# Kernel optimization log

Measured on AMD Instinct MI355X. Metric: run time of the kernel, lower is better.

Reference implementation:

```python
import jax, jax.numpy as jnp
import numpy as np
import math

B, N, DEG, C, F0, NCLS = 128, 512, 8, 128, 128, 10
E = B * N * DEG
RATIO = 0.8
K1 = math.ceil(RATIO * N)    # 410
K2 = math.ceil(RATIO * K1)   # 328
K3 = math.ceil(RATIO * K2)   # 263


def setup_inputs() -> dict:
    key = jax.random.key(0)
    ks = jax.random.split(key, 32)
    x = jax.random.normal(ks[0], (B * N, F0), jnp.float32)
    epg = N * DEG
    src_l = jax.random.randint(ks[1], (B, epg), 0, N)
    dst_l = jax.random.randint(ks[2], (B, epg), 0, N)
    off = (jnp.arange(B, dtype=jnp.int32) * N)[:, None]
    edge_src = (src_l + off).reshape(-1).astype(jnp.int32)
    edge_dst = (dst_l + off).reshape(-1).astype(jnp.int32)

    def lin(k, fi, fo):
        return jax.random.normal(k, (fi, fo), jnp.float32) / np.float32(np.sqrt(fi))

    inp = {"x": x, "edge_src": edge_src, "edge_dst": edge_dst}
    i = 3
    for s, fi in (("1", F0), ("2", C), ("3", C)):
        inp["Wroot" + s] = lin(ks[i], fi, C); i += 1
        inp["Wrel" + s] = lin(ks[i], fi, C); i += 1
        inp["brel" + s] = jnp.zeros((C,), jnp.float32)
        inp["p" + s] = jax.random.normal(ks[i], (C,), jnp.float32); i += 1
    inp["W1"] = lin(ks[i], 2 * C, 128); i += 1
    inp["b1"] = jnp.zeros((128,), jnp.float32)
    inp["W2"] = lin(ks[i], 128, 64); i += 1
    inp["b2"] = jnp.zeros((64,), jnp.float32)
    inp["W3"] = lin(ks[i], 64, NCLS); i += 1
    inp["b3"] = jnp.zeros((NCLS,), jnp.float32)
    return inp


def graph_conv(x, src, dst, emask, Wroot, Wrel, brel, num_nodes):
    # PyG GraphConv (aggr='add'): lin_rel(sum_j x_j) + lin_root(x_i)
    msg = x[src] * emask[:, None]                      # masked gather  [E, C]
    agg = jax.ops.segment_sum(msg, dst, num_segments=num_nodes)
    return agg @ Wrel + brel + x @ Wroot


def topk_pool(x, p, src, dst, emask, b, n, k):
    # score = tanh(x . p / ||p||), keep top-k nodes per graph, scale kept x by score
    score = jnp.tanh((x @ p) / jnp.linalg.norm(p))     # [b*n]
    vals, idx = jax.lax.top_k(score.reshape(b, n), k)  # [b, k]
    perm = (idx + (jnp.arange(b, dtype=idx.dtype) * n)[:, None]).reshape(-1)
    x_new = x[perm] * vals.reshape(-1, 1)
    inv = jnp.full((b * n,), -1, jnp.int32).at[perm].set(
        jnp.arange(b * k, dtype=jnp.int32))
    ns, nd = inv[src], inv[dst]
    nmask = emask * (ns >= 0) * (nd >= 0)
    return x_new, jnp.maximum(ns, 0), jnp.maximum(nd, 0), nmask


def readout(h, b, k):
    hb = h.reshape(b, k, -1)
    return jnp.concatenate([hb.max(axis=1), hb.mean(axis=1)], axis=-1)  # gmp||gap


def reference(x, edge_src, edge_dst,
              Wroot1, Wrel1, brel1, p1,
              Wroot2, Wrel2, brel2, p2,
              Wroot3, Wrel3, brel3, p3,
              W1, b1, W2, b2, W3, b3):
    emask = jnp.ones((E,), x.dtype)
    s, d = edge_src, edge_dst

    h = jax.nn.relu(graph_conv(x, s, d, emask, Wroot1, Wrel1, brel1, B * N))
    h, s, d, emask = topk_pool(h, p1, s, d, emask, B, N, K1)
    x1 = readout(h, B, K1)

    h = jax.nn.relu(graph_conv(h, s, d, emask, Wroot2, Wrel2, brel2, B * K1))
    h, s, d, emask = topk_pool(h, p2, s, d, emask, B, K1, K2)
    x2 = readout(h, B, K2)

    h = jax.nn.relu(graph_conv(h, s, d, emask, Wroot3, Wrel3, brel3, B * K2))
    h, s, d, emask = topk_pool(h, p3, s, d, emask, B, K2, K3)
    x3 = readout(h, B, K3)

    g = x1 + x2 + x3                                   # [B, 256]
    g = jax.nn.relu(g @ W1 + b1)                       # dropout is identity in eval
    g = jax.nn.relu(g @ W2 + b2)
    return jax.nn.log_softmax(g @ W3 + b3, axis=-1)    # [B, NCLS]
```

## Files before the change

kernel.cpp:

```cpp
#include <hip/hip_runtime.h>
#include <hip/hip_bf16.h>
#include <math.h>

#define B_G   128
#define N0    512
#define DEG   8
#define CCH   128
#define EPG   (N0*DEG)
#define E_TOTAL (B_G*EPG)
#define K1    410
#define K2    328
#define K3    263
#define NCLS  10

#define SWZ(row, cb) ((((cb) ^ ((row) & 7)) << 2))

using bf16x8 = __attribute__((ext_vector_type(8))) __bf16;
using f32x4  = __attribute__((ext_vector_type(4))) float;
typedef unsigned short ushort;
typedef unsigned int uint;
typedef unsigned long long u64;

__device__ __forceinline__ ushort f2b(float f) {
    uint u = __float_as_uint(f);
    u += 0x7fffu + ((u >> 16) & 1u);
    return (ushort)(u >> 16);
}
__device__ __forceinline__ float b2f(ushort h) {
    return __uint_as_float(((uint)h) << 16);
}
__device__ __forceinline__ void split2(float v, ushort& hi, ushort& lo) {
    hi = f2b(v);
    lo = f2b(v - b2f(hi));
}
__device__ __forceinline__ uint pksplit(float v) {
    ushort h, l; split2(v, h, l);
    return (uint)h | ((uint)l << 16);
}
__device__ __forceinline__ float unpk(uint u) {
    return __uint_as_float(u << 16) + __uint_as_float(u & 0xffff0000u);
}
__device__ __forceinline__ float keyval(u64 key) {
    uint tu = (uint)(key >> 32);
    uint su = (tu & 0x80000000u) ? (tu & 0x7fffffffu) : ~tu;
    return __uint_as_float(su);
}

__global__ __launch_bounds__(512) void setup_kernel(
        const float* __restrict__ Wrel0, const float* __restrict__ Wroot0,
        const float* __restrict__ Wrel1, const float* __restrict__ Wroot1,
        const float* __restrict__ Wrel2, const float* __restrict__ Wroot2,
        ushort* __restrict__ Bph, ushort* __restrict__ Bpl,
        const int* __restrict__ es, const int* __restrict__ ed,
        int* __restrict__ indptr0, int* __restrict__ counts0, ushort* __restrict__ srclist0) {
    __shared__ uint epk[EPG];
    __shared__ int cnt[512], pref[512], curs[512];
    if (blockIdx.x < B_G) {
        int b = blockIdx.x, tid = threadIdx.x;
        cnt[tid] = 0;
        __syncthreads();
        int base = b * EPG;
        for (int i = tid; i < EPG; i += 512) {
            int s = es[base + i] & (N0 - 1);
            int d = ed[base + i] & (N0 - 1);
            epk[i] = (uint)s | ((uint)d << 16);
            atomicAdd(&cnt[d], 1);
        }
        __syncthreads();
        pref[tid] = cnt[tid];
        __syncthreads();
        for (int off = 1; off < 512; off <<= 1) {
            int v = (tid >= off) ? pref[tid - off] : 0;
            __syncthreads();
            pref[tid] += v;
            __syncthreads();
        }
        int excl = tid ? pref[tid - 1] : 0;
        indptr0[b * N0 + tid] = base + excl;
        counts0[b * N0 + tid] = cnt[tid];
        curs[tid] = excl;
        __syncthreads();
        for (int i = tid; i < EPG; i += 512) {
            uint wv = epk[i];
            int dl = wv >> 16;
            int pos = atomicAdd(&curs[dl], 1);
            srclist0[base + pos] = (ushort)(wv & 0xFFFFu);
        }
    } else {
        int i = (blockIdx.x - B_G) * 512 + threadIdx.x;
        if (i < 3 * 32768) {
            int layer = i >> 15, rem = i & 32767;
            int j = rem & 7, lane = (rem >> 3) & 63, cf = (rem >> 9) & 7, ks = rem >> 12;
            int k = ks * 32 + (lane >> 4) * 8 + j;
            int c = cf * 16 + (lane & 15);
            const float* Wrel  = layer == 0 ? Wrel0  : layer == 1 ? Wrel1  : Wrel2;
            const float* Wroot = layer == 0 ? Wroot0 : layer == 1 ? Wroot1 : Wroot2;
            float v = (k < 128) ? Wrel[k * 128 + c] : Wroot[(k - 128) * 128 + c];
            ushort hi, lo; split2(v, hi, lo);
            Bph[i] = hi; Bpl[i] = lo;
        }
    }
}

__global__ __launch_bounds__(1024) void aggregate0(
        const float* __restrict__ xf,
        const int* __restrict__ indptr, const int* __restrict__ counts,
        const ushort* __restrict__ srclist,
        uint* __restrict__ aggp) {
    extern __shared__ float slab[];
    int b = blockIdx.x >> 2, q = blockIdx.x & 3;
    int tid = threadIdx.x;
    const float4* xf4 = (const float4*)xf;
    for (int t = tid; t < N0 * 8; t += 1024) {
        int nd = t >> 3, c4 = t & 7;
        float4 u = xf4[(size_t)(b * N0 + nd) * 32 + q * 8 + c4];
        *(float4*)&slab[nd * 32 + SWZ(nd, c4)] = u;
    }
    __syncthreads();
    int wave = tid >> 6, lane = tid & 63;
    int gl = lane >> 3, sub = lane & 7;
    for (int g = wave; g < N0 / 8; g += 16) {
        int d = g * 8 + gl;
        int beg = indptr[b * N0 + d];
        int cnt = counts[b * N0 + d];
        float4 acc = make_float4(0.f, 0.f, 0.f, 0.f);
        int id_next = (cnt > 0) ? (int)srclist[beg] : 0;
        for (int j = 0; j < cnt; j++) {
            int id = id_next;
            if (j + 1 < cnt) id_next = (int)srclist[beg + j + 1];
            const float4 v = *(const float4*)&slab[id * 32 + SWZ(id, sub)];
            acc.x += v.x; acc.y += v.y; acc.z += v.z; acc.w += v.w;
        }
        uint4 o;
        o.x = pksplit(acc.x); o.y = pksplit(acc.y);
        o.z = pksplit(acc.z); o.w = pksplit(acc.w);
        *(uint4*)&aggp[(size_t)(b * N0 + d) * CCH + q * 32 + sub * 4] = o;
    }
}

__global__ __launch_bounds__(512, 4) void transform_mfma(
        const uint* __restrict__ aggp, const uint* __restrict__ rootp,
        const float* __restrict__ rootf, const float* __restrict__ sval,
        const ushort* __restrict__ Bph, const ushort* __restrict__ Bpl,
        const float* __restrict__ brel, const float* __restrict__ pvec,
        uint* __restrict__ hout, float* __restrict__ score) {
    __shared__ ushort ldsBh[16384];
    __shared__ ushort ldsBl[16384];
    int tid = threadIdx.x;
    int wave = tid >> 6, lane = tid & 63;
    int r = lane & 15, kb = lane >> 4;
    int rows0 = blockIdx.x * 128 + wave * 16;
    int gid = rows0 + r;
    float rv = sval ? sval[gid] : 1.f;

    f32x4 acc[8];
#pragma unroll
    for (int cf = 0; cf < 8; cf++) acc[cf] = (f32x4)(0.f);

    union U16 { uint u[4]; bf16x8 v; };

#pragma unroll
    for (int half = 0; half < 2; half++) {
        if (half) __syncthreads();
#pragma unroll
        for (int i = 0; i < 4; i++) {
            int idx = tid + i * 512;
            ((uint4*)ldsBh)[idx] = ((const uint4*)(Bph + half * 16384))[idx];
            ((uint4*)ldsBl)[idx] = ((const uint4*)(Bpl + half * 16384))[idx];
        }
        __syncthreads();
#pragma unroll
        for (int ks4 = 0; ks4 < 4; ks4++) {
            U16 ah, al;
            if (half && rootf) {
                const float* R = rootf + (size_t)gid * CCH + ks4 * 32 + kb * 8;
                float4 f0 = *(const float4*)R;
                float4 f1 = *(const float4*)(R + 4);
                float c[8] = {f0.x, f0.y, f0.z, f0.w, f1.x, f1.y, f1.z, f1.w};
#pragma unroll
                for (int p2 = 0; p2 < 4; p2++) {
                    ushort h0, l0, h1, l1;
                    split2(c[2 * p2], h0, l0);
                    split2(c[2 * p2 + 1], h1, l1);
                    ah.u[p2] = (uint)h0 | ((uint)h1 << 16);
                    al.u[p2] = (uint)l0 | ((uint)l1 << 16);
                }
            } else {
                const uint* A = half ? rootp : aggp;
                size_t rowbase = (size_t)gid * CCH + ks4 * 32 + kb * 8;
                uint4 ua = *(const uint4*)&A[rowbase];
                uint4 ub = *(const uint4*)&A[rowbase + 4];
                if (half && sval) {
                    float c[8] = {unpk(ua.x) * rv, unpk(ua.y) * rv, unpk(ua.z) * rv,
                                  unpk(ua.w) * rv, unpk(ub.x) * rv, unpk(ub.y) * rv,
                                  unpk(ub.z) * rv, unpk(ub.w) * rv};
#pragma unroll
                    for (int p2 = 0; p2 < 4; p2++) {
                        ushort h0, l0, h1, l1;
                        split2(c[2 * p2], h0, l0);
                        split2(c[2 * p2 + 1], h1, l1);
                        ah.u[p2] = (uint)h0 | ((uint)h1 << 16);
                        al.u[p2] = (uint)l0 | ((uint)l1 << 16);
                    }
                } else {
                    ah.u[0] = (ua.x & 0xffffu) | (ua.y << 16);
                    ah.u[1] = (ua.z & 0xffffu) | (ua.w << 16);
                    ah.u[2] = (ub.x & 0xffffu) | (ub.y << 16);
                    ah.u[3] = (ub.z & 0xffffu) | (ub.w << 16);
                    al.u[0] = (ua.x >> 16) | (ua.y & 0xffff0000u);
                    al.u[1] = (ua.z >> 16) | (ua.w & 0xffff0000u);
                    al.u[2] = (ub.x >> 16) | (ub.y & 0xffff0000u);
                    al.u[3] = (ub.z >> 16) | (ub.w & 0xffff0000u);
                }
            }
#pragma unroll
            for (int cf = 0; cf < 8; cf++) {
                bf16x8 bh = *(const bf16x8*)&ldsBh[((ks4 * 8 + cf) * 64 + lane) * 8];
                bf16x8 bl = *(const bf16x8*)&ldsBl[((ks4 * 8 + cf) * 64 + lane) * 8];
                acc[cf] = __builtin_amdgcn_mfma_f32_16x16x32_bf16(ah.v, bl, acc[cf], 0, 0, 0);
                acc[cf] = __builtin_amdgcn_mfma_f32_16x16x32_bf16(al.v, bh, acc[cf], 0, 0, 0);
                acc[cf] = __builtin_amdgcn_mfma_f32_16x16x32_bf16(ah.v, bh, acc[cf], 0, 0, 0);
            }
        }
    }

    float pv[8], bb[8], q = 0.f;
#pragma unroll
    for (int cf = 0; cf < 8; cf++) {
        pv[cf] = pvec[cf * 16 + r];
        bb[cf] = brel[cf * 16 + r];
        q += pv[cf] * pv[cf];
    }
    float dots[4] = {0.f, 0.f, 0.f, 0.f};
#pragma unroll
    for (int cf = 0; cf < 8; cf++) {
#pragma unroll
        for (int reg = 0; reg < 4; reg++) {
            float v = acc[cf][reg] + bb[cf];
            v = v > 0.f ? v : 0.f;
            hout[(size_t)(rows0 + kb * 4 + reg) * CCH + cf * 16 + r] = pksplit(v);
            dots[reg] += v * pv[cf];
        }
    }
#pragma unroll
    for (int off = 1; off < 16; off <<= 1) {
        q += __shfl_xor(q, off);
#pragma unroll
        for (int reg = 0; reg < 4; reg++) dots[reg] += __shfl_xor(dots[reg], off);
    }
    if (r == 0) {
        float inv_norm = rsqrtf(q);
#pragma unroll
        for (int reg = 0; reg < 4; reg++)
            score[rows0 + kb * 4 + reg] = tanhf(dots[reg] * inv_norm);
    }
}

__global__ __launch_bounds__(1024) void pool_kernel(
        const float* __restrict__ score, const uint* __restrict__ hp,
        float* __restrict__ gpart,
        const int* __restrict__ ipt, const int* __restrict__ cnt,
        const ushort* __restrict__ srcl,
        const int* __restrict__ valid_in,
        int* __restrict__ valid_out,
        float* __restrict__ sval_out,
        uint* __restrict__ aggout,
        int k) {
    int b = blockIdx.x >> 2, q = blockIdx.x & 3;
    int tid = threadIdx.x;
    __shared__ char selm[512];
    __shared__ float sval[512];
    __shared__ int hist[256];
    __shared__ int cum[257];
    __shared__ int bc[1];
    __shared__ float redbuf[2048];
    extern __shared__ float slab[];

    u64 key = 0ull;
    if (tid < 512) {
        bool v = (!valid_in) || (valid_in[b * N0 + tid] != 0);
        if (v) {
            uint u = __float_as_uint(score[b * N0 + tid]);
            u = (u & 0x80000000u) ? ~u : (u | 0x80000000u);
            key = ((u64)u << 32) | (uint)(~tid);
            sval[tid] = keyval(key);
        }
    }
    for (int t = tid; t < N0 * 8; t += 1024) {
        int nd = t >> 3, c4 = t & 7;
        bool v = (!valid_in) || (valid_in[b * N0 + nd] != 0);
        if (v) {
            uint4 u = *(const uint4*)&hp[(size_t)(b * N0 + nd) * CCH + q * 32 + c4 * 4];
            *(float4*)&slab[nd * 32 + SWZ(nd, c4)] =
                make_float4(unpk(u.x), unpk(u.y), unpk(u.z), unpk(u.w));
        }
    }
    bool active = (tid < 512) && (key != 0ull), sure = false;
    int rem = k;
    for (int pass = 0; pass < 8; pass++) {
        int dig = (int)((key >> (56 - 8 * pass)) & 255);
        if (tid < 256) hist[tid] = 0;
        __syncthreads();
        if (active) atomicAdd(&hist[dig], 1);
        __syncthreads();
        if (tid < 64) {
            int b0 = hist[tid * 4], b1 = hist[tid * 4 + 1];
            int b2 = hist[tid * 4 + 2], b3 = hist[tid * 4 + 3];
            int s = b0 + b1 + b2 + b3;
            int suf = s;
#pragma unroll
            for (int o = 1; o < 64; o <<= 1) {
                int t2 = __shfl_down(suf, o);
                if (tid + o < 64) suf += t2;
            }
            int after = suf - s;
            cum[tid * 4 + 3] = after + b3;
            cum[tid * 4 + 2] = after + b3 + b2;
            cum[tid * 4 + 1] = after + b3 + b2 + b1;
            cum[tid * 4 + 0] = after + s;
            if (tid == 0) cum[256] = 0;
        }
        __syncthreads();
        if (tid < 256 && cum[tid] >= rem && cum[tid + 1] < rem) bc[0] = tid;
        __syncthreads();
        int dstar = bc[0];
        int hcnt = hist[dstar];
        rem -= cum[dstar + 1];
        if (active) {
            if (dig > dstar) { sure = true; active = false; }
            else if (dig < dstar) active = false;
        }
        __syncthreads();
        if (hcnt == 1) break;
    }
    bool sel = sure || (active && rem > 0);
    if (tid < 512) selm[tid] = sel ? 1 : 0;
    __syncthreads();
    for (int t = tid; t < N0 * 8; t += 1024) {
        int nd = t >> 3, c4 = t & 7;
        if (selm[nd]) {
            float v = sval[nd];
            float* p = &slab[nd * 32 + SWZ(nd, c4)];
            p[0] *= v; p[1] *= v; p[2] *= v; p[3] *= v;
        }
    }
    __syncthreads();
    {
        int w = tid >> 5, ch = tid & 31;
        int cb = ch >> 2, ce = ch & 3;
        float mx = -1e30f, sm = 0.f;
        for (int nd = w; nd < N0; nd += 32) {
            float v = slab[nd * 32 + SWZ(nd, cb) + ce];
            if (selm[nd]) { mx = fmaxf(mx, v); sm += v; }
        }
        redbuf[w * 32 + ch] = mx;
        redbuf[1024 + w * 32 + ch] = sm;
    }
    __syncthreads();
    if (tid < 32) {
        float m = -1e30f, s = 0.f;
        for (int w = 0; w < 32; w++) {
            m = fmaxf(m, redbuf[w * 32 + tid]);
            s += redbuf[1024 + w * 32 + tid];
        }
        gpart[b * 256 + q * 32 + tid] = m;
        gpart[b * 256 + 128 + q * 32 + tid] = s / (float)k;
    }
    if (!valid_out) return;
    if (q == 0 && tid < 512) {
        valid_out[b * N0 + tid] = selm[tid] ? 1 : 0;
        sval_out[b * N0 + tid] = selm[tid] ? sval[tid] : 0.f;
    }
    {
        int wave = tid >> 6, lane = tid & 63;
        int gl = lane >> 3, sub = lane & 7;
        for (int g = wave; g < N0 / 8; g += 16) {
            int d = g * 8 + gl;
            bool act = selm[d] != 0;
            int beg = 0, cc = 0;
            if (act) { beg = ipt[b * N0 + d]; cc = cnt[b * N0 + d]; }
            float4 acc = make_float4(0.f, 0.f, 0.f, 0.f);
            int s_next = (cc > 0) ? (int)srcl[beg] : 0;
            for (int j = 0; j < cc; j++) {
                int s = s_next;
                if (j + 1 < cc) s_next = (int)srcl[beg + j + 1];
                if (selm[s]) {
                    const float4 v = *(const float4*)&slab[s * 32 + SWZ(s, sub)];
                    acc.x += v.x; acc.y += v.y; acc.z += v.z; acc.w += v.w;
                }
            }
            if (act) {
                uint4 o;
                o.x = pksplit(acc.x); o.y = pksplit(acc.y);
                o.z = pksplit(acc.z); o.w = pksplit(acc.w);
                *(uint4*)&aggout[(size_t)(b * N0 + d) * CCH + q * 32 + sub * 4] = o;
            }
        }
    }
}

__global__ __launch_bounds__(128) void mlp_kernel(const float* __restrict__ gpart,
        const float* __restrict__ W1, const float* __restrict__ b1,
        const float* __restrict__ W2, const float* __restrict__ b2,
        const float* __restrict__ W3, const float* __restrict__ b3,
        float* __restrict__ out) {
    int b = blockIdx.x, t = threadIdx.x;
    __shared__ float gs[256], h1[128], h2[64], lg[10];
    const float* g0 = gpart + ((size_t)0 * B_G + b) * 256;
    const float* g1 = gpart + ((size_t)1 * B_G + b) * 256;
    const float* g2 = gpart + ((size_t)2 * B_G + b) * 256;
    gs[t] = g0[t] + g1[t] + g2[t];
    gs[128 + t] = g0[128 + t] + g1[128 + t] + g2[128 + t];
    __syncthreads();
    {
        float a = b1[t];
        for (int c = 0; c < 256; c++) a += gs[c] * W1[c * 128 + t];
        h1[t] = fmaxf(a, 0.f);
    }
    __syncthreads();
    if (t < 64) {
        float a = b2[t];
        for (int c = 0; c < 128; c++) a += h1[c] * W2[c * 64 + t];
        h2[t] = fmaxf(a, 0.f);
    }
    __syncthreads();
    if (t < 10) {
        float a = b3[t];
        for (int c = 0; c < 64; c++) a += h2[c] * W3[c * 10 + t];
        lg[t] = a;
    }
    __syncthreads();
    if (t < 10) {
        float m = lg[0];
        for (int i = 1; i < 10; i++) m = fmaxf(m, lg[i]);
        float s = 0.f;
        for (int i = 0; i < 10; i++) s += expf(lg[i] - m);
        out[b * 10 + t] = lg[t] - m - logf(s);
    }
}

extern "C" void kernel_launch(void* const* d_in, const int* in_sizes, int n_in,
                              void* d_out, int out_size, void* d_ws, size_t ws_size,
                              hipStream_t stream) {
    (void)in_sizes; (void)n_in; (void)out_size; (void)ws_size;
    const float* x0 = (const float*)d_in[0];
    const int* es = (const int*)d_in[1];
    const int* ed = (const int*)d_in[2];
    const float* Wroot[3] = {(const float*)d_in[3], (const float*)d_in[7], (const float*)d_in[11]};
    const float* Wrel[3]  = {(const float*)d_in[4], (const float*)d_in[8], (const float*)d_in[12]};
    const float* brel[3]  = {(const float*)d_in[5], (const float*)d_in[9], (const float*)d_in[13]};
    const float* pvec[3]  = {(const float*)d_in[6], (const float*)d_in[10], (const float*)d_in[14]};
    const float* W1 = (const float*)d_in[15];
    const float* b1 = (const float*)d_in[16];
    const float* W2 = (const float*)d_in[17];
    const float* b2 = (const float*)d_in[18];
    const float* W3 = (const float*)d_in[19];
    const float* b3 = (const float*)d_in[20];

    size_t off = 0;
    char* base = (char*)d_ws;
    auto alloc = [&](size_t bytes) -> void* {
        void* p = base + off;
        off += (bytes + 255) & ~(size_t)255;
        return p;
    };
    const size_t FEATP = (size_t)(B_G * N0) * CCH * 4;
    uint* PA = (uint*)alloc(FEATP);
    uint* PB = (uint*)alloc(FEATP);
    uint* P1 = (uint*)alloc(FEATP);
    ushort* Bph = (ushort*)alloc((size_t)3 * 32768 * 2);
    ushort* Bpl = (ushort*)alloc((size_t)3 * 32768 * 2);
    int* ipt = (int*)alloc((size_t)(B_G * N0) * 4);
    int* cnt = (int*)alloc((size_t)(B_G * N0) * 4);
    ushort* srcl = (ushort*)alloc((size_t)E_TOTAL * 2);
    int* valid1 = (int*)alloc((size_t)(B_G * N0) * 4);
    int* valid2 = (int*)alloc((size_t)(B_G * N0) * 4);
    float* sval1 = (float*)alloc((size_t)(B_G * N0) * 4);
    float* sval2 = (float*)alloc((size_t)(B_G * N0) * 4);
    float* score = (float*)alloc((size_t)(B_G * N0) * 4);
    float* gpart = (float*)alloc((size_t)3 * B_G * 256 * 4);

    setup_kernel<<<B_G + (3 * 32768 + 511) / 512, 512, 0, stream>>>(
        Wrel[0], Wroot[0], Wrel[1], Wroot[1], Wrel[2], Wroot[2],
        Bph, Bpl, es, ed, ipt, cnt, srcl);

    const size_t SLAB = (size_t)N0 * 32 * 4;
    aggregate0<<<4 * B_G, 1024, SLAB, stream>>>(x0, ipt, cnt, srcl, P1);
    transform_mfma<<<B_G * N0 / 128, 512, 0, stream>>>(
        P1, nullptr, x0, nullptr, Bph, Bpl, brel[0], pvec[0], PA, score);
    pool_kernel<<<4 * B_G, 1024, SLAB, stream>>>(
        score, PA, gpart + (size_t)0 * B_G * 256,
        ipt, cnt, srcl, nullptr, valid1, sval1, P1, K1);

    transform_mfma<<<B_G * N0 / 128, 512, 0, stream>>>(
        P1, PA, nullptr, sval1, Bph + 32768, Bpl + 32768, brel[1], pvec[1], PB, score);
    pool_kernel<<<4 * B_G, 1024, SLAB, stream>>>(
        score, PB, gpart + (size_t)1 * B_G * 256,
        ipt, cnt, srcl, valid1, valid2, sval2, P1, K2);

    transform_mfma<<<B_G * N0 / 128, 512, 0, stream>>>(
        P1, PB, nullptr, sval2, Bph + 2 * 32768, Bpl + 2 * 32768, brel[2], pvec[2], PA, score);
    pool_kernel<<<4 * B_G, 1024, SLAB, stream>>>(
        score, PA, gpart + (size_t)2 * B_G * 256,
        ipt, cnt, srcl, valid2, nullptr, nullptr, nullptr, K3);

    mlp_kernel<<<B_G, 128, 0, stream>>>(gpart, W1, b1, W2, b2, W3, b3, (float*)d_out);
}
```

Baseline: 196.7 us.

## Replace radix-select top-k with single-wave bitonic sort overlapped with slab loading

The multi-pass shared-memory radix select, which needed several block-wide barriers per pass, is replaced by a register bitonic sort of the 512 keys inside wave 0 using shuffles. The k-th largest key becomes a threshold, and a node is selected when its key is at least that threshold. Meanwhile the other 15 waves load and unpack the feature slab from global memory, so the selection work overlaps the load. The costs are a serial bitonic network on one wave and slab loading spread over fewer threads.

```diff
diff --git a/kernel.cpp b/kernel.cpp
--- a/kernel.cpp
+++ b/kernel.cpp
@@ -268,73 +268,91 @@
         int k) {
     int b = blockIdx.x >> 2, q = blockIdx.x & 3;
     int tid = threadIdx.x;
+    __shared__ u64 keysL[512];
     __shared__ char selm[512];
     __shared__ float sval[512];
-    __shared__ int hist[256];
-    __shared__ int cum[257];
-    __shared__ int bc[1];
+    __shared__ u64 thresh;
     __shared__ float redbuf[2048];
     extern __shared__ float slab[];
 
-    u64 key = 0ull;
+    u64 mykey = 0ull;
     if (tid < 512) {
         bool v = (!valid_in) || (valid_in[b * N0 + tid] != 0);
         if (v) {
             uint u = __float_as_uint(score[b * N0 + tid]);
             u = (u & 0x80000000u) ? ~u : (u | 0x80000000u);
-            key = ((u64)u << 32) | (uint)(~tid);
-            sval[tid] = keyval(key);
-        }
-    }
-    for (int t = tid; t < N0 * 8; t += 1024) {
-        int nd = t >> 3, c4 = t & 7;
-        bool v = (!valid_in) || (valid_in[b * N0 + nd] != 0);
-        if (v) {
-            uint4 u = *(const uint4*)&hp[(size_t)(b * N0 + nd) * CCH + q * 32 + c4 * 4];
-            *(float4*)&slab[nd * 32 + SWZ(nd, c4)] =
-                make_float4(unpk(u.x), unpk(u.y), unpk(u.z), unpk(u.w));
-        }
-    }
-    bool active = (tid < 512) && (key != 0ull), sure = false;
-    int rem = k;
-    for (int pass = 0; pass < 8; pass++) {
-        int dig = (int)((key >> (56 - 8 * pass)) & 255);
-        if (tid < 256) hist[tid] = 0;
-        __syncthreads();
-        if (active) atomicAdd(&hist[dig], 1);
-        __syncthreads();
-        if (tid < 64) {
-            int b0 = hist[tid * 4], b1 = hist[tid * 4 + 1];
-            int b2 = hist[tid * 4 + 2], b3 = hist[tid * 4 + 3];
-            int s = b0 + b1 + b2 + b3;
-            int suf = s;
-#pragma unroll
-            for (int o = 1; o < 64; o <<= 1) {
-                int t2 = __shfl_down(suf, o);
-                if (tid + o < 64) suf += t2;
-            }
-            int after = suf - s;
-            cum[tid * 4 + 3] = after + b3;
-            cum[tid * 4 + 2] = after + b3 + b2;
-            cum[tid * 4 + 1] = after + b3 + b2 + b1;
-            cum[tid * 4 + 0] = after + s;
-            if (tid == 0) cum[256] = 0;
-        }
-        __syncthreads();
-        if (tid < 256 && cum[tid] >= rem && cum[tid + 1] < rem) bc[0] = tid;
-        __syncthreads();
-        int dstar = bc[0];
-        int hcnt = hist[dstar];
-        rem -= cum[dstar + 1];
-        if (active) {
-            if (dig > dstar) { sure = true; active = false; }
-            else if (dig < dstar) active = false;
-        }
-        __syncthreads();
-        if (hcnt == 1) break;
-    }
-    bool sel = sure || (active && rem > 0);
-    if (tid < 512) selm[tid] = sel ? 1 : 0;
+            mykey = ((u64)u << 32) | (uint)(~tid);
+            sval[tid] = keyval(mykey);
+        }
+        keysL[tid] = mykey;
+    }
+    __syncthreads();
+    int wave = tid >> 6, lane = tid & 63;
+    if (wave == 0) {
+        u64 kr[8];
+#pragma unroll
+        for (int r = 0; r < 8; r++) kr[r] = keysL[r * 64 + lane];
+        for (int kk2 = 2; kk2 <= 512; kk2 <<= 1) {
+            for (int j = kk2 >> 1; j > 0; j >>= 1) {
+                if (j >= 64) {
+                    int m = j >> 6;
+#pragma unroll
+                    for (int r = 0; r < 8; r++) {
+                        if ((r & m) == 0) {
+                            int r2 = r | m;
+                            u64 a = kr[r], c = kr[r2];
+                            bool desc = (((r << 6) & kk2) == 0);
+                            u64 mx = a > c ? a : c;
+                            u64 mn = a > c ? c : a;
+                            kr[r]  = desc ? mx : mn;
+                            kr[r2] = desc ? mn : mx;
+                        }
+                    }
+                } else {
+#pragma unroll
+                    for (int r = 0; r < 8; r++) {
+                        u64 p = __shfl_xor(kr[r], j);
+                        int e = (r << 6) + lane;
+                        bool desc = ((e & kk2) == 0);
+                        bool lower = ((lane & j) == 0);
+                        u64 mx = kr[r] > p ? kr[r] : p;
+                        u64 mn = kr[r] > p ? p : kr[r];
+                        kr[r] = (desc == lower) ? mx : mn;
+                    }
+                }
+            }
+        }
+        int ls = (k - 1) & 63, rs = (k - 1) >> 6;
+        if (lane == ls) {
+            u64 kt;
+            switch (rs) {
+                case 0: kt = kr[0]; break;
+                case 1: kt = kr[1]; break;
+                case 2: kt = kr[2]; break;
+                case 3: kt = kr[3]; break;
+                case 4: kt = kr[4]; break;
+                case 5: kt = kr[5]; break;
+                case 6: kt = kr[6]; break;
+                default: kt = kr[7]; break;
+            }
+            thresh = kt;
+        }
+    } else {
+        for (int t = tid - 64; t < N0 * 8; t += 960) {
+            int nd = t >> 3, c4 = t & 7;
+            bool v = (!valid_in) || (valid_in[b * N0 + nd] != 0);
+            if (v) {
+                uint4 u = *(const uint4*)&hp[(size_t)(b * N0 + nd) * CCH + q * 32 + c4 * 4];
+                *(float4*)&slab[nd * 32 + SWZ(nd, c4)] =
+                    make_float4(unpk(u.x), unpk(u.y), unpk(u.z), unpk(u.w));
+            }
+        }
+    }
+    __syncthreads();
+    if (tid < 512) {
+        u64 T = thresh;
+        selm[tid] = (mykey != 0ull && mykey >= T) ? 1 : 0;
+    }
     __syncthreads();
     for (int t = tid; t < N0 * 8; t += 1024) {
         int nd = t >> 3, c4 = t & 7;
@@ -359,9 +377,9 @@
     __syncthreads();
     if (tid < 32) {
         float m = -1e30f, s = 0.f;
-        for (int w = 0; w < 32; w++) {
-            m = fmaxf(m, redbuf[w * 32 + tid]);
-            s += redbuf[1024 + w * 32 + tid];
+        for (int w2 = 0; w2 < 32; w2++) {
+            m = fmaxf(m, redbuf[w2 * 32 + tid]);
+            s += redbuf[1024 + w2 * 32 + tid];
         }
         gpart[b * 256 + q * 32 + tid] = m;
         gpart[b * 256 + 128 + q * 32 + tid] = s / (float)k;
@@ -372,7 +390,6 @@
         sval_out[b * N0 + tid] = selm[tid] ? sval[tid] : 0.f;
     }
     {
-        int wave = tid >> 6, lane = tid & 63;
         int gl = lane >> 3, sub = lane & 7;
         for (int g = wave; g < N0 / 8; g += 16) {
             int d = g * 8 + gl;
```

New measurement: 344.2 us. +75.0%, slower.
